# Kernel tuning notes

Measured on AMD Instinct MI355X. Metric: run time of the kernel, lower is better.

Reference implementation:

```python
import jax, jax.numpy as jnp
import numpy as np

# --- config (matches init_kwargs) ---
HID = 2048      # hidden_size
H = 16          # num_attention_heads
D_NOPE = 128    # qk_nope_head_dim
D_ROPE = 64     # qk_rope_head_dim
D_Q = D_NOPE + D_ROPE  # 192
D_V = 128       # v_head_dim
QR = 1536       # q_lora_rank
KVR = 512       # kv_lora_rank
PH = 16         # pattern_heads
PD = HID // PH  # 128
THETA = 10000.0
EPS = 1e-6


def rmsnorm(x, w):
    var = jnp.mean(jnp.square(x), axis=-1, keepdims=True)
    return x * jax.lax.rsqrt(var + EPS) * w


def rope_cos_sin(seq_len):
    inv_freq = 1.0 / (THETA ** (jnp.arange(0, D_ROPE, 2, dtype=jnp.float32) / D_ROPE))
    t = jnp.arange(seq_len, dtype=jnp.float32)
    freqs = jnp.outer(t, inv_freq)            # [S, D_ROPE/2]
    emb = jnp.concatenate([freqs, freqs], -1)  # [S, D_ROPE]
    return jnp.cos(emb), jnp.sin(emb)


def rotate_half(x):
    x1, x2 = jnp.split(x, 2, axis=-1)
    return jnp.concatenate([-x2, x1], axis=-1)


def apply_rope(x, cos, sin):
    # x: [B, H, S, D_ROPE]; cos/sin: [S, D_ROPE]
    return x * cos[None, None] + rotate_half(x) * sin[None, None]


def setup_inputs() -> dict:
    key = jax.random.key(0)
    ks = jax.random.split(key, 12)
    def w(k, shape):
        return (jax.random.normal(k, shape, jnp.float32) / np.sqrt(shape[-1])).astype(jnp.float32)
    B, S = 2, 1024
    return {
        "hidden_states": jax.random.normal(ks[0], (B, S, HID), jnp.float32),
        "q_a_w": w(ks[1], (QR, HID)),
        "q_a_ln_w": jnp.ones((QR,), jnp.float32),
        "q_b_w": w(ks[2], (H * D_Q, QR)),
        "kv_a_w": w(ks[3], (KVR + H * D_ROPE, HID)),
        "kv_a_ln_w": jnp.ones((KVR,), jnp.float32),
        "kv_b_w": w(ks[4], (H * (D_NOPE + D_V), KVR)),
        "o_w": w(ks[5], (HID, H * D_V)),
        "sp_q_w": w(ks[6], (HID, HID)),
        "sp_k_w": w(ks[7], (HID, HID)),
        "sp_v_w": w(ks[8], (HID, HID)),
        "sp_o_w": w(ks[9], (HID, HID)),
        "gate_w": w(ks[10], (2, HID)),
        "gate_b": jnp.zeros((2,), jnp.float32),
    }


def reference(hidden_states, q_a_w, q_a_ln_w, q_b_w, kv_a_w, kv_a_ln_w, kv_b_w,
              o_w, sp_q_w, sp_k_w, sp_v_w, sp_o_w, gate_w, gate_b):
    b, s, _ = hidden_states.shape
    dt = hidden_states.dtype

    # ---- main MLA path ----
    q_mid = rmsnorm(hidden_states @ q_a_w.T, q_a_ln_w)                      # [B,S,QR]
    q = (q_mid @ q_b_w.T).reshape(b, s, H, D_Q).transpose(0, 2, 1, 3)       # [B,H,S,Dq]
    q_nope, q_pe = q[..., :D_NOPE], q[..., D_NOPE:]

    kv_a = hidden_states @ kv_a_w.T                                         # [B,S,KVR+H*Dr]
    kv_lora, k_pe_flat = kv_a[..., :KVR], kv_a[..., KVR:]
    k_pe = k_pe_flat.reshape(b, s, H, D_ROPE).transpose(0, 2, 1, 3)         # [B,H,S,Dr]

    kv = (rmsnorm(kv_lora, kv_a_ln_w) @ kv_b_w.T)
    kv = kv.reshape(b, s, H, D_NOPE + D_V).transpose(0, 2, 1, 3)            # [B,H,S,Dn+Dv]
    k_nope, v = kv[..., :D_NOPE], kv[..., D_NOPE:]

    cos, sin = rope_cos_sin(s)
    q_pe = apply_rope(q_pe, cos, sin)
    k_pe = apply_rope(k_pe, cos, sin)

    qf = jnp.concatenate([q_nope, q_pe], -1)                                # [B,H,S,Dq]
    kf = jnp.concatenate([k_nope, k_pe], -1)

    scale = D_Q ** -0.5
    scores = jnp.einsum('bhqd,bhkd->bhqk', qf, kf) * scale
    probs = jax.nn.softmax(scores.astype(jnp.float32), axis=-1).astype(dt)
    ctx = jnp.einsum('bhqk,bhkd->bhqd', probs, v)                           # [B,H,S,Dv]
    main_out = ctx.transpose(0, 2, 1, 3).reshape(b, s, H * D_V) @ o_w.T     # [B,S,HID]

    # ---- self pattern path (standard MHA on hidden_states) ----
    def split_heads(x):
        return x.reshape(b, s, PH, PD).transpose(0, 2, 1, 3)
    pq = split_heads(hidden_states @ sp_q_w.T)
    pk = split_heads(hidden_states @ sp_k_w.T)
    pv = split_heads(hidden_states @ sp_v_w.T)
    p_scores = jnp.einsum('bhqd,bhkd->bhqk', pq, pk) * (PD ** -0.5)
    p_probs = jax.nn.softmax(p_scores.astype(jnp.float32), axis=-1).astype(dt)
    p_ctx = jnp.einsum('bhqk,bhkd->bhqd', p_probs, pv)
    pattern_out = p_ctx.transpose(0, 2, 1, 3).reshape(b, s, HID) @ sp_o_w.T

    # ---- learned gate over paths ----
    gates = jax.nn.softmax(hidden_states @ gate_w.T + gate_b, axis=-1)      # [B,S,2]
    return gates[..., 0:1] * main_out + gates[..., 1:2] * pattern_out
```

## Files before the change

kernel.cpp:

```cpp
#include <hip/hip_runtime.h>
#include <math.h>
#include <stdint.h>

#define HIDN  2048
#define NH    16
#define DNOPE 128
#define DROPE 64
#define DQ    192
#define DV    128
#define QRANK 1536
#define KVRANK 512
#define SEQ   1024
#define NBATCH 2
#define NTOK  (NBATCH*SEQ)
#define EPSV  1e-6f

typedef unsigned short u16;
typedef unsigned int   u32;
typedef __attribute__((ext_vector_type(8))) short  short8;
typedef __attribute__((ext_vector_type(8))) unsigned short ushort8;
typedef __attribute__((ext_vector_type(4))) float  f32x4;

__device__ __forceinline__ u16 f2b(float f) {
    u32 u = __float_as_uint(f);
    u = (u + 0x7fffu + ((u >> 16) & 1u)) >> 16;
    return (u16)u;
}
__device__ __forceinline__ float b2f(u16 h) {
    return __uint_as_float(((u32)h) << 16);
}

__device__ __forceinline__ void async_copy16(const u16* g, u16* l) {
    __builtin_amdgcn_global_load_lds(
        (const __attribute__((address_space(1))) u32*)g,
        (__attribute__((address_space(3))) u32*)l,
        16, 0, 0);
}

__device__ __forceinline__ int swz(int r, int c) { return r * 4 + (c ^ ((r >> 1) & 3)); }

struct CastArgs {
    const float* s[10];
    u16* d[10];
    int cum[11];
};
__global__ __launch_bounds__(256)
void cast_all(CastArgs a, int total_chunks)
{
    int c = blockIdx.x * 256 + threadIdx.x;
    if (c >= total_chunks) return;
    int seg = 0;
    #pragma unroll
    for (int i = 1; i < 10; ++i) seg += (c >= a.cum[i]) ? 1 : 0;
    int local = c - a.cum[seg];
    const float* src = a.s[seg] + (size_t)local * 8;
    u16* dst = a.d[seg] + (size_t)local * 8;
    float4 x = *(const float4*)(src);
    float4 y = *(const float4*)(src + 4);
    ushort8 o;
    o[0]=f2b(x.x); o[1]=f2b(x.y); o[2]=f2b(x.z); o[3]=f2b(x.w);
    o[4]=f2b(y.x); o[5]=f2b(y.y); o[6]=f2b(y.z); o[7]=f2b(y.w);
    *(ushort8*)(dst) = o;
}

struct GemmSeg {
    const u16* X; const u16* W;
    float* Cf; u16* Cb; u16* Cb2; u16* Cb3;
    int K; int ldx; int ldc; int mode; int bx0;
};
struct GemmArgs { GemmSeg seg[3]; int nseg; };

__global__ __launch_bounds__(256)
void gemm_multi(GemmArgs a)
{
    __shared__ __align__(16) u16 As[2 * 4096];
    __shared__ __align__(16) u16 Bs[2 * 4096];
    int s = 0;
    if (a.nseg > 1 && (int)blockIdx.x >= a.seg[1].bx0) s = 1;
    if (a.nseg > 2 && (int)blockIdx.x >= a.seg[2].bx0) s = 2;
    const GemmSeg g = a.seg[s];

    const int tid = threadIdx.x;
    const int bn = ((int)blockIdx.x - g.bx0) * 128;
    const int bm = blockIdx.y * 128;
    const int lane = tid & 63, wv = tid >> 6;
    const int lm = lane & 15, lq = lane >> 4;
    const int wm = (wv >> 1) * 64, wn = (wv & 1) * 64;
    const int ldx = g.ldx, K = g.K;
    const u16* Xp = g.X;
    const u16* Wp = g.W;

    auto stage = [&](int kt, int buf) {
        int k0 = kt * 32;
        #pragma unroll
        for (int it = 0; it < 2; ++it) {
            int base = wv * 64 + it * 256;
            int slot = base + lane;
            int r = slot >> 2, c = (slot & 3) ^ ((r >> 1) & 3);
            async_copy16(Xp + (size_t)(bm + r) * ldx + k0 + c * 8,
                         As + buf * 4096 + base * 8);
            async_copy16(Wp + (size_t)(bn + r) * K + k0 + c * 8,
                         Bs + buf * 4096 + base * 8);
        }
    };

    f32x4 acc[4][4] = {};
    const int niter = K >> 5;
    stage(0, 0);
    for (int kt = 0; kt < niter; ++kt) {
        int cur = kt & 1;
        __syncthreads();
        if (kt + 1 < niter) stage(kt + 1, cur ^ 1);
        const u16* Ab = As + cur * 4096;
        const u16* Bb = Bs + cur * 4096;
        short8 af[4], bf[4];
        #pragma unroll
        for (int mt = 0; mt < 4; ++mt) {
            int R = wm + mt * 16 + lm;
            af[mt] = *(const short8*)(Ab + swz(R, lq) * 8);
        }
        #pragma unroll
        for (int nt = 0; nt < 4; ++nt) {
            int R = wn + nt * 16 + lm;
            bf[nt] = *(const short8*)(Bb + swz(R, lq) * 8);
        }
        #pragma unroll
        for (int mt = 0; mt < 4; ++mt)
            #pragma unroll
            for (int nt = 0; nt < 4; ++nt)
                acc[mt][nt] = __builtin_amdgcn_mfma_f32_16x16x32_bf16(
                    af[mt], bf[nt], acc[mt][nt], 0, 0, 0);
    }

    const int mode = g.mode;
    #pragma unroll
    for (int mt = 0; mt < 4; ++mt) {
        int token0 = bm + wm + mt * 16 + lq * 4;
        #pragma unroll
        for (int nt = 0; nt < 4; ++nt) {
            int feat = bn + wn + nt * 16 + lm;
            #pragma unroll
            for (int i = 0; i < 4; ++i) {
                float v = acc[mt][nt][i];
                int tok = token0 + i;
                int b2 = tok >> 10, s2 = tok & (SEQ - 1);
                if (mode == 0) {
                    g.Cf[(size_t)tok * g.ldc + feat] = v;
                } else if (mode == 5) {
                    g.Cb[(size_t)tok * g.ldc + feat] = f2b(v);
                } else if (mode == 1) {
                    int h2 = feat / DQ, d = feat - h2 * DQ;
                    g.Cb[((size_t)((b2 * NH + h2) * SEQ + s2)) * DQ + d] = f2b(v);
                } else if (mode == 3) {
                    int h2 = feat >> 8, c = feat & 255;
                    if (c < 128)
                        g.Cb[((size_t)((b2 * NH + h2) * SEQ + s2)) * DQ + c] = f2b(v);
                    else
                        g.Cb2[((size_t)((b2 * NH + h2) * 128 + (c - 128))) * SEQ + s2] = f2b(v);
                } else {
                    int wsel = feat >> 11;
                    int f2 = feat & 2047;
                    int h2 = f2 >> 7, d = f2 & 127;
                    if (wsel == 0)
                        g.Cb[((size_t)((b2 * NH + h2) * SEQ + s2)) * 128 + d] = f2b(v);
                    else if (wsel == 1)
                        g.Cb2[((size_t)((b2 * NH + h2) * SEQ + s2)) * 128 + d] = f2b(v);
                    else
                        g.Cb3[((size_t)((b2 * NH + h2) * 128 + d)) * SEQ + s2] = f2b(v);
                }
            }
        }
    }
}

__global__ __launch_bounds__(256)
void rmsnorm_fused(u16* __restrict__ amid, const float* __restrict__ qw,
                   const float* __restrict__ kvw)
{
    int row = blockIdx.x;
    u16* x; const float* w; int D;
    if (row < NTOK) { x = amid + (size_t)row * 3072;            w = qw;  D = QRANK; }
    else            { x = amid + (size_t)(row - NTOK) * 3072 + QRANK; w = kvw; D = KVRANK; }
    float ss = 0.f;
    for (int d = threadIdx.x; d < D; d += 256) { float v = b2f(x[d]); ss += v * v; }
    __shared__ float red[256];
    red[threadIdx.x] = ss;
    __syncthreads();
    for (int off = 128; off > 0; off >>= 1) {
        if (threadIdx.x < off) red[threadIdx.x] += red[threadIdx.x + off];
        __syncthreads();
    }
    float inv = rsqrtf(red[0] / (float)D + EPSV);
    for (int d = threadIdx.x; d < D; d += 256)
        x[d] = f2b(b2f(x[d]) * inv * w[d]);
}

__global__ __launch_bounds__(256)
void rope_fused(u16* __restrict__ qf, const u16* __restrict__ amid,
                u16* __restrict__ kf)
{
    int t = blockIdx.x * 256 + threadIdx.x;
    bool isq = t < (1 << 20);
    int tt = isq ? t : t - (1 << 20);
    int i = tt & 31, s = (tt >> 5) & (SEQ - 1), bh = tt >> 15;
    float inv_freq = powf(10000.f, -(float)i / 32.f);
    float ang = (float)s * inv_freq;
    float c, sn; sincosf(ang, &sn, &c);
    if (isq) {
        u16* p = qf + ((size_t)bh * SEQ + s) * DQ;
        float x1 = b2f(p[DNOPE + i]), x2 = b2f(p[DNOPE + 32 + i]);
        p[DNOPE + i]      = f2b(x1 * c - x2 * sn);
        p[DNOPE + 32 + i] = f2b(x2 * c + x1 * sn);
    } else {
        int h = bh & (NH - 1), bb = bh >> 4;
        const u16* src = amid + ((size_t)(bb * SEQ + s)) * 3072 + (QRANK + KVRANK) + h * DROPE;
        float x1 = b2f(src[i]), x2 = b2f(src[32 + i]);
        u16* dst = kf + ((size_t)bh * SEQ + s) * DQ + DNOPE;
        dst[i]      = f2b(x1 * c - x2 * sn);
        dst[32 + i] = f2b(x2 * c + x1 * sn);
    }
}

template<int DQK>
__device__ __forceinline__
void flash_body(const u16* __restrict__ Q, const u16* __restrict__ Kf,
                const u16* __restrict__ Vt, u16* __restrict__ ctx_out,
                float scale, u16* Ks, u16* Vs, u16* Ps, int qt, int h, int bb)
{
    constexpr int KSZ  = 32 * DQK;
    constexpr int VSZ  = 32 * 128;
    constexpr int NKIT = DQK / 64;
    constexpr int NT   = SEQ / 32;
    const int tid = threadIdx.x, lane = tid & 63, wv = tid >> 6;
    const int lm = lane & 15, lq = lane >> 4;
    const size_t bh = (size_t)bb * NH + h;
    const u16* Qb = Q + (bh * SEQ + qt * 64 + wv * 16) * (size_t)DQK;
    const u16* Kb = Kf + bh * SEQ * (size_t)DQK;
    const u16* Vb = Vt + bh * (size_t)128 * SEQ;

    short8 qfrag[DQK / 32];
    #pragma unroll
    for (int ks = 0; ks < DQK / 32; ++ks)
        qfrag[ks] = *(const short8*)(Qb + lm * DQK + ks * 32 + lq * 8);

    auto stage = [&](int kt, int buf) {
        #pragma unroll
        for (int it = 0; it < NKIT; ++it) {
            int base = it * 256 + wv * 64;
            int slot = base + lane;
            int plane = slot >> 7, rem = slot & 127;
            int key = rem >> 2, c = (rem & 3) ^ ((key >> 1) & 3);
            async_copy16(Kb + (size_t)(kt * 32 + key) * DQK + plane * 32 + c * 8,
                         Ks + buf * KSZ + base * 8);
        }
        #pragma unroll
        for (int it = 0; it < 2; ++it) {
            int base = it * 256 + wv * 64;
            int slot = base + lane;
            int d = slot >> 2, c = (slot & 3) ^ ((d >> 1) & 3);
            async_copy16(Vb + (size_t)d * SEQ + kt * 32 + c * 8,
                         Vs + buf * VSZ + base * 8);
        }
    };

    float m_i[4], l_i[4];
    #pragma unroll
    for (int i = 0; i < 4; ++i) { m_i[i] = -INFINITY; l_i[i] = 0.f; }
    f32x4 oacc[8] = {};

    stage(0, 0);
    for (int kt = 0; kt < NT; ++kt) {
        int cur = kt & 1;
        __syncthreads();
        if (kt + 1 < NT) stage(kt + 1, cur ^ 1);
        const u16* Kc = Ks + cur * KSZ;
        const u16* Vc = Vs + cur * VSZ;

        f32x4 sacc[2] = {};
        #pragma unroll
        for (int kb = 0; kb < 2; ++kb)
            #pragma unroll
            for (int ks = 0; ks < DQK / 32; ++ks) {
                int R = kb * 16 + lm;
                short8 kfr = *(const short8*)(Kc + ks * 1024 + swz(R, lq) * 8);
                sacc[kb] = __builtin_amdgcn_mfma_f32_16x16x32_bf16(
                    qfrag[ks], kfr, sacc[kb], 0, 0, 0);
            }

        float p0[4], p1[4], alpha[4];
        #pragma unroll
        for (int i = 0; i < 4; ++i) {
            float s0 = sacc[0][i] * scale, s1 = sacc[1][i] * scale;
            float mx = fmaxf(s0, s1);
            mx = fmaxf(mx, __shfl_xor(mx, 1));
            mx = fmaxf(mx, __shfl_xor(mx, 2));
            mx = fmaxf(mx, __shfl_xor(mx, 4));
            mx = fmaxf(mx, __shfl_xor(mx, 8));
            float mnew = fmaxf(m_i[i], mx);
            p0[i] = __expf(s0 - mnew);
            p1[i] = __expf(s1 - mnew);
            float sum = p0[i] + p1[i];
            sum += __shfl_xor(sum, 1);
            sum += __shfl_xor(sum, 2);
            sum += __shfl_xor(sum, 4);
            sum += __shfl_xor(sum, 8);
            alpha[i] = __expf(m_i[i] - mnew);
            l_i[i] = l_i[i] * alpha[i] + sum;
            m_i[i] = mnew;
        }

        u16* Pw = Ps + wv * 640;
        #pragma unroll
        for (int i = 0; i < 4; ++i) {
            Pw[(lq * 4 + i) * 40 + lm]      = f2b(p0[i]);
            Pw[(lq * 4 + i) * 40 + 16 + lm] = f2b(p1[i]);
        }
        short8 pfrag = *(const short8*)(Pw + lm * 40 + lq * 8);

        #pragma unroll
        for (int nt = 0; nt < 8; ++nt) {
            #pragma unroll
            for (int i = 0; i < 4; ++i) oacc[nt][i] *= alpha[i];
            int R = nt * 16 + lm;
            short8 vfr = *(const short8*)(Vc + swz(R, lq) * 8);
            oacc[nt] = __builtin_amdgcn_mfma_f32_16x16x32_bf16(
                pfrag, vfr, oacc[nt], 0, 0, 0);
        }
    }

    int s0 = qt * 64 + wv * 16 + lq * 4;
    #pragma unroll
    for (int i = 0; i < 4; ++i) {
        float inv = 1.f / l_i[i];
        u16* dst = ctx_out + ((size_t)(bb * SEQ + s0 + i) * NH + h) * 128;
        #pragma unroll
        for (int nt = 0; nt < 8; ++nt)
            dst[nt * 16 + lm] = f2b(oacc[nt][i] * inv);
    }
}

__global__ __launch_bounds__(256, 3)
void flash_fused(const u16* qf, const u16* kf, const u16* Vtg, u16* ctx,
                 const u16* pq, const u16* pk, const u16* pvt, u16* p_ctx,
                 float scale_main, float scale_pat)
{
    __shared__ __align__(16) u16 Ks[2 * 32 * DQ];
    __shared__ __align__(16) u16 Vs[2 * 32 * 128];
    __shared__ __align__(16) u16 Ps[4 * 16 * 40];
    int h = blockIdx.x, qtb = blockIdx.y, bb = blockIdx.z;
    if (qtb < 16)
        flash_body<DQ>(qf, kf, Vtg, ctx, scale_main, Ks, Vs, Ps, qtb, h, bb);
    else
        flash_body<128>(pq, pk, pvt, p_ctx, scale_pat, Ks, Vs, Ps, qtb - 16, h, bb);
}

__global__ __launch_bounds__(256)
void gate_combine(const float* __restrict__ x, const float* __restrict__ gw,
                  const float* __restrict__ gb,
                  const float* __restrict__ mo, const float* __restrict__ po,
                  float* __restrict__ out)
{
    const int tok = blockIdx.x;
    const float* xr = x + (size_t)tok * HIDN;
    float d0 = 0.f, d1 = 0.f;
    for (int i = threadIdx.x; i < HIDN; i += 256) {
        float v = xr[i];
        d0 += v * gw[i];
        d1 += v * gw[HIDN + i];
    }
    __shared__ float r0[256], r1[256];
    r0[threadIdx.x] = d0; r1[threadIdx.x] = d1;
    __syncthreads();
    for (int off = 128; off > 0; off >>= 1) {
        if (threadIdx.x < off) {
            r0[threadIdx.x] += r0[threadIdx.x + off];
            r1[threadIdx.x] += r1[threadIdx.x + off];
        }
        __syncthreads();
    }
    float l0 = r0[0] + gb[0], l1 = r1[0] + gb[1];
    float m = fmaxf(l0, l1);
    float e0 = __expf(l0 - m), e1 = __expf(l1 - m);
    float g0 = e0 / (e0 + e1), g1 = e1 / (e0 + e1);
    const float* mr = mo + (size_t)tok * HIDN;
    const float* pr = po + (size_t)tok * HIDN;
    float* orow = out + (size_t)tok * HIDN;
    for (int i = threadIdx.x; i < HIDN; i += 256)
        orow[i] = g0 * mr[i] + g1 * pr[i];
}

extern "C" void kernel_launch(void* const* d_in, const int* in_sizes, int n_in,
                              void* d_out, int out_size, void* d_ws, size_t ws_size,
                              hipStream_t stream)
{
    const float* X        = (const float*)d_in[0];
    const float* q_a_w    = (const float*)d_in[1];
    const float* q_a_ln_w = (const float*)d_in[2];
    const float* q_b_w    = (const float*)d_in[3];
    const float* kv_a_w   = (const float*)d_in[4];
    const float* kv_a_ln_w= (const float*)d_in[5];
    const float* kv_b_w   = (const float*)d_in[6];
    const float* o_w      = (const float*)d_in[7];
    const float* sp_q_w   = (const float*)d_in[8];
    const float* sp_k_w   = (const float*)d_in[9];
    const float* sp_v_w   = (const float*)d_in[10];
    const float* sp_o_w   = (const float*)d_in[11];
    const float* gate_w   = (const float*)d_in[12];
    const float* gate_b   = (const float*)d_in[13];
    float* out = (float*)d_out;

    char* p = (char*)d_ws;
    auto alloc = [&](size_t bytes) -> char* {
        char* r = p; p += (bytes + 255) & ~(size_t)255; return r;
    };
    u16* amid      = (u16*)alloc((size_t)NTOK * 3072 * 2);
    u16* Xb        = (u16*)alloc((size_t)NTOK * HIDN * 2);
    u16* aw_b      = (u16*)alloc((size_t)3072 * HIDN * 2);
    u16* q_b_wb    = (u16*)alloc((size_t)NH * DQ * QRANK * 2);
    u16* kv_b_wb   = (u16*)alloc((size_t)NH * 256 * KVRANK * 2);
    u16* o_wb      = (u16*)alloc((size_t)HIDN * HIDN * 2);
    u16* spqkv_wb  = (u16*)alloc((size_t)3 * HIDN * HIDN * 2);
    u16* sp_o_wb   = (u16*)alloc((size_t)HIDN * HIDN * 2);
    u16* qf        = (u16*)alloc((size_t)NTOK * NH * DQ * 2);
    u16* kf        = (u16*)alloc((size_t)NTOK * NH * DQ * 2);
    u16* Vtg       = (u16*)alloc((size_t)NBATCH * NH * 128 * SEQ * 2);
    u16* pq        = (u16*)alloc((size_t)NTOK * HIDN * 2);
    u16* pk        = (u16*)alloc((size_t)NTOK * HIDN * 2);
    u16* pvt    = aw_b;
    u16* ctx    = q_b_wb;
    u16* p_ctx  = spqkv_wb;
    float* patout = (float*)qf;

    dim3 blk(256);

    CastArgs ca;
    const float* srcs[10] = {X, q_a_w, kv_a_w, q_b_w, kv_b_w, o_w,
                             sp_q_w, sp_k_w, sp_v_w, sp_o_w};
    u16* dsts[10] = {Xb, aw_b, aw_b + (size_t)QRANK * HIDN, q_b_wb, kv_b_wb, o_wb,
                     spqkv_wb, spqkv_wb + (size_t)HIDN * HIDN,
                     spqkv_wb + (size_t)2 * HIDN * HIDN, sp_o_wb};
    int ns[10] = {NTOK * HIDN, QRANK * HIDN, 1536 * HIDN, NH * DQ * QRANK,
                  NH * 256 * KVRANK, HIDN * HIDN, HIDN * HIDN, HIDN * HIDN,
                  HIDN * HIDN, HIDN * HIDN};
    int cum = 0;
    for (int i = 0; i < 10; ++i) {
        ca.s[i] = srcs[i]; ca.d[i] = dsts[i];
        ca.cum[i] = cum; cum += ns[i] / 8;
    }
    ca.cum[10] = cum;
    cast_all<<<dim3((cum + 255) / 256), blk, 0, stream>>>(ca, cum);

    {
        GemmArgs ga = {};
        ga.nseg = 1;
        ga.seg[0] = {Xb, aw_b, nullptr, amid, nullptr, nullptr,
                     HIDN, HIDN, 3072, 5, 0};
        gemm_multi<<<dim3(24, 16), blk, 0, stream>>>(ga);
    }

    rmsnorm_fused<<<dim3(2 * NTOK), blk, 0, stream>>>(amid, q_a_ln_w, kv_a_ln_w);

    {
        GemmArgs ga = {};
        ga.nseg = 3;
        ga.seg[0] = {amid, q_b_wb, nullptr, qf, nullptr, nullptr,
                     QRANK, 3072, 0, 1, 0};
        ga.seg[1] = {amid + QRANK, kv_b_wb, nullptr, kf, Vtg, nullptr,
                     KVRANK, 3072, 0, 3, 24};
        ga.seg[2] = {Xb, spqkv_wb, nullptr, pq, pk, pvt,
                     HIDN, HIDN, 0, 4, 56};
        gemm_multi<<<dim3(104, 16), blk, 0, stream>>>(ga);
    }

    rope_fused<<<dim3(8192), blk, 0, stream>>>(qf, amid, kf);

    flash_fused<<<dim3(NH, 32, NBATCH), blk, 0, stream>>>(
        qf, kf, Vtg, ctx, pq, pk, pvt, p_ctx,
        1.0f / sqrtf((float)DQ), 1.0f / sqrtf(128.0f));

    {
        GemmArgs ga = {};
        ga.nseg = 2;
        ga.seg[0] = {ctx, o_wb, out, nullptr, nullptr, nullptr,
                     HIDN, HIDN, HIDN, 0, 0};
        ga.seg[1] = {p_ctx, sp_o_wb, patout, nullptr, nullptr, nullptr,
                     HIDN, HIDN, HIDN, 0, 16};
        gemm_multi<<<dim3(32, 16), blk, 0, stream>>>(ga);
    }

    gate_combine<<<dim3(NTOK), blk, 0, stream>>>(X, gate_w, gate_b, out, patout, out);
}
```

Measured before the change: 602.6 us.

## Add lazy softmax rescaling, MFMA priority hints, and reorder GEMM segments

In the flash attention inner loop, the running max and output accumulator are now rescaled only when some row's new max exceeds the old one by more than a threshold, checked wave-wide. This skips the per-tile exp and accumulator multiplies in most iterations, at the cost of letting unnormalized values grow by up to e^8 in fp32. MFMA sections are wrapped in s_setprio hints so they get scheduling priority over other waves. The multi-segment GEMM is reordered to put the large K=2048 pattern QKV segment first, which should improve tail balancing, and the RoPE powf is replaced with an exp2f of a precomputed constant.

```diff
diff --git a/kernel.cpp b/kernel.cpp
--- a/kernel.cpp
+++ b/kernel.cpp
@@ -203,7 +203,7 @@
     bool isq = t < (1 << 20);
     int tt = isq ? t : t - (1 << 20);
     int i = tt & 31, s = (tt >> 5) & (SEQ - 1), bh = tt >> 15;
-    float inv_freq = powf(10000.f, -(float)i / 32.f);
+    float inv_freq = exp2f((float)i * -0.41524101186f);
     float ang = (float)s * inv_freq;
     float c, sn; sincosf(ang, &sn, &c);
     if (isq) {
@@ -277,6 +277,7 @@
         const u16* Vc = Vs + cur * VSZ;
 
         f32x4 sacc[2] = {};
+        __builtin_amdgcn_s_setprio(1);
         #pragma unroll
         for (int kb = 0; kb < 2; ++kb)
             #pragma unroll
@@ -286,27 +287,44 @@
                 sacc[kb] = __builtin_amdgcn_mfma_f32_16x16x32_bf16(
                     qfrag[ks], kfr, sacc[kb], 0, 0, 0);
             }
-
-        float p0[4], p1[4], alpha[4];
+        __builtin_amdgcn_s_setprio(0);
+
+        float s0v[4], s1v[4], mx[4];
         #pragma unroll
         for (int i = 0; i < 4; ++i) {
             float s0 = sacc[0][i] * scale, s1 = sacc[1][i] * scale;
-            float mx = fmaxf(s0, s1);
-            mx = fmaxf(mx, __shfl_xor(mx, 1));
-            mx = fmaxf(mx, __shfl_xor(mx, 2));
-            mx = fmaxf(mx, __shfl_xor(mx, 4));
-            mx = fmaxf(mx, __shfl_xor(mx, 8));
-            float mnew = fmaxf(m_i[i], mx);
-            p0[i] = __expf(s0 - mnew);
-            p1[i] = __expf(s1 - mnew);
+            float m2 = fmaxf(s0, s1);
+            m2 = fmaxf(m2, __shfl_xor(m2, 1));
+            m2 = fmaxf(m2, __shfl_xor(m2, 2));
+            m2 = fmaxf(m2, __shfl_xor(m2, 4));
+            m2 = fmaxf(m2, __shfl_xor(m2, 8));
+            s0v[i] = s0; s1v[i] = s1; mx[i] = m2;
+        }
+        bool need = false;
+        #pragma unroll
+        for (int i = 0; i < 4; ++i) need |= (mx[i] > m_i[i] + 8.f);
+        need = __any(need);
+        float alpha[4];
+        if (need) {
+            #pragma unroll
+            for (int i = 0; i < 4; ++i) {
+                float mnew = fmaxf(m_i[i], mx[i]);
+                alpha[i] = __expf(m_i[i] - mnew);
+                m_i[i] = mnew;
+                l_i[i] *= alpha[i];
+            }
+        }
+        float p0[4], p1[4];
+        #pragma unroll
+        for (int i = 0; i < 4; ++i) {
+            p0[i] = __expf(s0v[i] - m_i[i]);
+            p1[i] = __expf(s1v[i] - m_i[i]);
             float sum = p0[i] + p1[i];
             sum += __shfl_xor(sum, 1);
             sum += __shfl_xor(sum, 2);
             sum += __shfl_xor(sum, 4);
             sum += __shfl_xor(sum, 8);
-            alpha[i] = __expf(m_i[i] - mnew);
-            l_i[i] = l_i[i] * alpha[i] + sum;
-            m_i[i] = mnew;
+            l_i[i] += sum;
         }
 
         u16* Pw = Ps + wv * 640;
@@ -317,15 +335,21 @@
         }
         short8 pfrag = *(const short8*)(Pw + lm * 40 + lq * 8);
 
+        if (need) {
+            #pragma unroll
+            for (int nt = 0; nt < 8; ++nt)
+                #pragma unroll
+                for (int i = 0; i < 4; ++i) oacc[nt][i] *= alpha[i];
+        }
+        __builtin_amdgcn_s_setprio(1);
         #pragma unroll
         for (int nt = 0; nt < 8; ++nt) {
-            #pragma unroll
-            for (int i = 0; i < 4; ++i) oacc[nt][i] *= alpha[i];
             int R = nt * 16 + lm;
             short8 vfr = *(const short8*)(Vc + swz(R, lq) * 8);
             oacc[nt] = __builtin_amdgcn_mfma_f32_16x16x32_bf16(
                 pfrag, vfr, oacc[nt], 0, 0, 0);
         }
+        __builtin_amdgcn_s_setprio(0);
     }
 
     int s0 = qt * 64 + wv * 16 + lq * 4;
@@ -463,12 +487,12 @@
     {
         GemmArgs ga = {};
         ga.nseg = 3;
-        ga.seg[0] = {amid, q_b_wb, nullptr, qf, nullptr, nullptr,
-                     QRANK, 3072, 0, 1, 0};
-        ga.seg[1] = {amid + QRANK, kv_b_wb, nullptr, kf, Vtg, nullptr,
-                     KVRANK, 3072, 0, 3, 24};
-        ga.seg[2] = {Xb, spqkv_wb, nullptr, pq, pk, pvt,
-                     HIDN, HIDN, 0, 4, 56};
+        ga.seg[0] = {Xb, spqkv_wb, nullptr, pq, pk, pvt,
+                     HIDN, HIDN, 0, 4, 0};
+        ga.seg[1] = {amid, q_b_wb, nullptr, qf, nullptr, nullptr,
+                     QRANK, 3072, 0, 1, 48};
+        ga.seg[2] = {amid + QRANK, kv_b_wb, nullptr, kf, Vtg, nullptr,
+                     KVRANK, 3072, 0, 3, 72};
         gemm_multi<<<dim3(104, 16), blk, 0, stream>>>(ga);
     }
 
```

Measured after the change: 598.9 us. No clear change (-0.6%).
